# Kernel optimization log

Hardware: AMD Instinct MI355X
Metric: run time of the kernel (lower is better)

The kernel has to match this reference:

```python
import jax, jax.numpy as jnp
import numpy as np

N = 50000   # nodes
E = 600000  # edges
D = 128     # node_input_dim
H = 128     # hidden_dim
A = 200000  # number of valid actions


def setup_inputs() -> dict:
    key = jax.random.key(0)
    ks = jax.random.split(key, 8)
    x = jax.random.normal(ks[0], (N, D), dtype=jnp.float32)
    edge_index = jax.random.randint(ks[1], (2, E), 0, N, dtype=jnp.int64)
    valid_actions = jax.random.randint(ks[2], (A, 2), 0, N, dtype=jnp.int64)
    # GCNConv uses glorot-style init for weight, zeros/uniform for bias; exact init is irrelevant for correctness
    s1 = 1.0 / np.sqrt(D)
    sH = 1.0 / np.sqrt(H)
    s2 = 1.0 / np.sqrt(2 * H)
    W1 = jax.random.uniform(ks[3], (D, H), jnp.float32, -s1, s1)
    b1 = jax.random.uniform(ks[4], (H,), jnp.float32, -s1, s1)
    W2 = jax.random.uniform(ks[5], (H, H), jnp.float32, -sH, sH)
    b2 = jax.random.uniform(ks[6], (H,), jnp.float32, -sH, sH)
    Wq = jax.random.uniform(ks[7], (2 * H, 1), jnp.float32, -s2, s2)
    bq = jnp.zeros((1,), jnp.float32)
    return {"x": x, "edge_index": edge_index, "valid_actions": valid_actions,
            "W1": W1, "b1": b1, "W2": W2, "b2": b2, "Wq": Wq, "bq": bq}


def _gcn_conv(h, src, dst, norm, W, b, n_nodes):
    # PyG GCNConv: x' = D^{-1/2} (A + I) D^{-1/2} X W + b
    h = h @ W                              # [N, H]
    msg = h[src] * norm[:, None]           # [E+N, H] gather + scale
    out = jax.ops.segment_sum(msg, dst, num_segments=n_nodes)  # scatter-add
    return out + b


def reference(x, edge_index, valid_actions, W1, b1, W2, b2, Wq, bq):
    n = x.shape[0]
    loops = jnp.arange(n, dtype=edge_index.dtype)
    src = jnp.concatenate([edge_index[0], loops])  # self-loops appended
    dst = jnp.concatenate([edge_index[1], loops])
    # symmetric normalization from in-degree of A+I (unit edge weights)
    deg = jax.ops.segment_sum(jnp.ones_like(dst, x.dtype), dst, num_segments=n)
    dis = jnp.where(deg > 0, jax.lax.rsqrt(deg), 0.0)
    norm = dis[src] * dis[dst]             # [E+N]

    h = jax.nn.relu(_gcn_conv(x, src, dst, norm, W1, b1, n))
    h = jax.nn.relu(_gcn_conv(h, src, dst, norm, W2, b2, n))

    # batched gather-concat-linear replacing the per-action Python loop
    pair = jnp.concatenate([h[valid_actions[:, 0]], h[valid_actions[:, 1]]], axis=-1)  # [A, 2H]
    q = pair @ Wq + bq                     # [A, 1]
    return q.reshape(-1)                   # torch.cat of A scalars -> [A]
```

## Files before the change

kernel.cpp:

```cpp
#include <hip/hip_runtime.h>
#include <hip/hip_bf16.h>

#define HDIM 128

typedef __attribute__((ext_vector_type(8))) short bf16x8_t;
typedef __attribute__((ext_vector_type(4))) float f32x4_t;

__device__ inline unsigned short bf16_rne(float x) {
    union { __hip_bfloat16 b; unsigned short u; } cv;
    cv.b = __float2bfloat16(x);
    return cv.u;
}
__device__ inline void split2(float x, unsigned short& h, unsigned short& l) {
    h = bf16_rne(x);
    l = bf16_rne(x - __uint_as_float((unsigned int)h << 16));
}

__global__ void deg_count_k(const int* __restrict__ dst, int* __restrict__ deg, int E) {
    int i = blockIdx.x * blockDim.x + threadIdx.x;
    if (i < E) atomicAdd(&deg[dst[i]], 1);
}

__global__ void scan_part_k(const int* __restrict__ deg, int* __restrict__ incl,
                            int* __restrict__ blocksum, int N) {
    __shared__ int s[256];
    const int tid = threadIdx.x;
    const int i = blockIdx.x * 256 + tid;
    int v = (i < N) ? deg[i] : 0;
    s[tid] = v;
    __syncthreads();
    #pragma unroll
    for (int off = 1; off < 256; off <<= 1) {
        int t = (tid >= off) ? s[tid - off] : 0;
        __syncthreads();
        s[tid] += t;
        __syncthreads();
    }
    if (i < N) incl[i] = s[tid];
    if (tid == 255) blocksum[blockIdx.x] = s[255];
}

__global__ void scan_final_k(const int* __restrict__ deg, const int* __restrict__ incl,
                             const int* __restrict__ blocksum, int* __restrict__ rowptr,
                             float* __restrict__ dis, int N, int E, int NB) {
    __shared__ int s[256];
    const int tid = threadIdx.x, bid = blockIdx.x;
    const int i = bid * 256 + tid;
    const int v = (tid < NB) ? blocksum[tid] : 0;
    s[tid] = v;
    __syncthreads();
    #pragma unroll
    for (int off = 1; off < 256; off <<= 1) {
        int t = (tid >= off) ? s[tid - off] : 0;
        __syncthreads();
        s[tid] += t;
        __syncthreads();
    }
    const int excl = s[bid] - blocksum[bid];
    if (i < N) {
        rowptr[i] = excl + incl[i] - deg[i];
        dis[i] = rsqrtf((float)deg[i] + 1.0f);
    }
    if (i == 0) rowptr[N] = E;
}

__global__ void fill_csr_k(const int* __restrict__ src, const int* __restrict__ dst,
                           const int* __restrict__ rowptr, int* __restrict__ cursor,
                           int* __restrict__ csr, int E) {
    int e = blockIdx.x * blockDim.x + threadIdx.x;
    if (e < E) {
        const int d = dst[e];
        const int pos = rowptr[d] + atomicAdd(&cursor[d], 1);
        csr[pos] = src[e];
    }
}

__global__ void pack_w2_k(const float* __restrict__ W1, const float* __restrict__ W2,
                          unsigned short* __restrict__ Wp1, unsigned short* __restrict__ Wp2) {
    const int idx = blockIdx.x * 256 + threadIdx.x;
    const float* W = (idx < 16384) ? W1 : W2;
    unsigned short* hi = (idx < 16384) ? Wp1 : Wp2;
    const int id = idx & 16383;
    const int frag = id >> 9;
    const int r = id & 511;
    const int lane = r >> 3, j = r & 7;
    const int c = frag & 7, sfrag = frag >> 3;
    const int col = (c << 4) | (lane & 15);
    const int k = (sfrag << 5) + ((lane >> 4) << 3) + j;
    unsigned short h, l;
    split2(W[k * HDIM + col], h, l);
    hi[id] = h;
    hi[id + 16384] = l;
}

__global__ __launch_bounds__(512, 4) void mfma_gemm_k(
    const float* __restrict__ X, const unsigned short* __restrict__ Wp,
    const float* __restrict__ dis, float* __restrict__ hs, int N) {
    __shared__ __align__(16) unsigned short wlds[32768];
    const int tid = threadIdx.x;
    {
        const float4* wsrc = reinterpret_cast<const float4*>(Wp);
        float4* wdst = reinterpret_cast<float4*>(wlds);
        #pragma unroll
        for (int i = 0; i < 8; ++i) wdst[tid + i * 512] = wsrc[tid + i * 512];
    }
    __syncthreads();

    const int wave = tid >> 6, lane = tid & 63;
    const int row0 = (blockIdx.x << 7) + (wave << 4);
    if (row0 >= N) return;
    const int lrow = lane & 15;
    const int kgrp = (lane >> 4) << 3;

    const long abase = ((long)(row0 + lrow) << 7) + kgrp;

    f32x4_t acc[8];
    #pragma unroll
    for (int c = 0; c < 8; ++c) acc[c] = (f32x4_t){0.f, 0.f, 0.f, 0.f};

    #pragma unroll
    for (int s = 0; s < 4; ++s) {
        const float4 a0 = *reinterpret_cast<const float4*>(X + abase + (s << 5));
        const float4 a1 = *reinterpret_cast<const float4*>(X + abase + (s << 5) + 4);
        const float xv[8] = {a0.x, a0.y, a0.z, a0.w, a1.x, a1.y, a1.z, a1.w};
        bf16x8_t ah, al;
        #pragma unroll
        for (int j = 0; j < 8; ++j) {
            unsigned short h, l;
            split2(xv[j], h, l);
            ah[j] = (short)h;
            al[j] = (short)l;
        }
        #pragma unroll
        for (int c = 0; c < 8; ++c) {
            const int fo = (((s << 3) + c) << 9) + (lane << 3);
            const bf16x8_t bh = *reinterpret_cast<const bf16x8_t*>(wlds + fo);
            const bf16x8_t bl = *reinterpret_cast<const bf16x8_t*>(wlds + 16384 + fo);
            acc[c] = __builtin_amdgcn_mfma_f32_16x16x32_bf16(ah, bh, acc[c], 0, 0, 0);
            acc[c] = __builtin_amdgcn_mfma_f32_16x16x32_bf16(al, bh, acc[c], 0, 0, 0);
            acc[c] = __builtin_amdgcn_mfma_f32_16x16x32_bf16(ah, bl, acc[c], 0, 0, 0);
        }
    }

    const int rbase = row0 + ((lane >> 4) << 2);
    float d[4];
    #pragma unroll
    for (int i = 0; i < 4; ++i) d[i] = dis[rbase + i];
    #pragma unroll
    for (int c = 0; c < 8; ++c) {
        const int col = (c << 4) | lrow;
        #pragma unroll
        for (int i = 0; i < 4; ++i)
            hs[((long)(rbase + i) << 7) + col] = acc[c][i] * d[i];
    }
}

template<bool PROJ>
__global__ __launch_bounds__(256) void gather_agg_k(
    const int* __restrict__ rowptr, const int* __restrict__ csr,
    const float* __restrict__ hs, const float* __restrict__ dis,
    const float* __restrict__ b, float* __restrict__ o,
    const float* __restrict__ Wq, float* __restrict__ pu, float* __restrict__ pv, int N) {
    const int lane = threadIdx.x & 63;
    const int wid = (int)((blockIdx.x * (long)blockDim.x + threadIdx.x) >> 6);
    const int nw = (int)(((long)gridDim.x * blockDim.x) >> 6);
    const float2 bb = *reinterpret_cast<const float2*>(&b[lane * 2]);
    float2 wu = {0.f, 0.f}, wv = {0.f, 0.f};
    if constexpr (PROJ) {
        wu = *reinterpret_cast<const float2*>(&Wq[lane * 2]);
        wv = *reinterpret_cast<const float2*>(&Wq[HDIM + lane * 2]);
    }
    const int loff = lane * 2;
    for (int n = wid; n < N; n += nw) {
        const int r0 = rowptr[n], r1 = rowptr[n + 1];
        float2 acc = *reinterpret_cast<const float2*>(&hs[((long)n << 7) + loff]);
        float2 acc2 = {0.f, 0.f};
        int e = r0;
        for (; e + 8 <= r1; e += 8) {
            const int s0 = csr[e],     s1 = csr[e + 1], s2 = csr[e + 2], s3 = csr[e + 3];
            const int s4 = csr[e + 4], s5 = csr[e + 5], s6 = csr[e + 6], s7 = csr[e + 7];
            const float2 v0 = *reinterpret_cast<const float2*>(&hs[((long)s0 << 7) + loff]);
            const float2 v1 = *reinterpret_cast<const float2*>(&hs[((long)s1 << 7) + loff]);
            const float2 v2 = *reinterpret_cast<const float2*>(&hs[((long)s2 << 7) + loff]);
            const float2 v3 = *reinterpret_cast<const float2*>(&hs[((long)s3 << 7) + loff]);
            const float2 v4 = *reinterpret_cast<const float2*>(&hs[((long)s4 << 7) + loff]);
            const float2 v5 = *reinterpret_cast<const float2*>(&hs[((long)s5 << 7) + loff]);
            const float2 v6 = *reinterpret_cast<const float2*>(&hs[((long)s6 << 7) + loff]);
            const float2 v7 = *reinterpret_cast<const float2*>(&hs[((long)s7 << 7) + loff]);
            acc.x  += v0.x + v1.x;  acc.y  += v0.y + v1.y;
            acc2.x += v2.x + v3.x;  acc2.y += v2.y + v3.y;
            acc.x  += v4.x + v5.x;  acc.y  += v4.y + v5.y;
            acc2.x += v6.x + v7.x;  acc2.y += v6.y + v7.y;
        }
        for (; e + 2 <= r1; e += 2) {
            const int s0 = csr[e], s1 = csr[e + 1];
            const float2 v0 = *reinterpret_cast<const float2*>(&hs[((long)s0 << 7) + loff]);
            const float2 v1 = *reinterpret_cast<const float2*>(&hs[((long)s1 << 7) + loff]);
            acc.x += v0.x + v1.x;
            acc.y += v0.y + v1.y;
        }
        if (e < r1) {
            const int s0 = csr[e];
            const float2 v0 = *reinterpret_cast<const float2*>(&hs[((long)s0 << 7) + loff]);
            acc.x += v0.x;
            acc.y += v0.y;
        }
        acc.x += acc2.x;
        acc.y += acc2.y;
        const float dv = dis[n];
        const float o0 = fmaxf(fmaf(acc.x, dv, bb.x), 0.f);
        const float o1 = fmaxf(fmaf(acc.y, dv, bb.y), 0.f);
        if constexpr (!PROJ) {
            float2 ov = {o0, o1};
            *reinterpret_cast<float2*>(o + ((long)n << 7) + loff) = ov;
        } else {
            float su = o0 * wu.x + o1 * wu.y;
            float sv = o0 * wv.x + o1 * wv.y;
            #pragma unroll
            for (int off = 32; off > 0; off >>= 1) {
                su += __shfl_down(su, off, 64);
                sv += __shfl_down(sv, off, 64);
            }
            if (lane == 0) {
                pu[n] = su;
                pv[n] = sv;
            }
        }
    }
}

__global__ __launch_bounds__(256) void qhead_k(
    const float* __restrict__ pu, const float* __restrict__ pv,
    const int* __restrict__ va, const float* __restrict__ bq,
    float* __restrict__ out, int A) {
    const float bqv = bq[0];
    int i = blockIdx.x * blockDim.x + threadIdx.x;
    const int stride = gridDim.x * blockDim.x;
    for (; i < A; i += stride) {
        const int2 uv = reinterpret_cast<const int2*>(va)[i];
        out[i] = pu[uv.x] + pv[uv.y] + bqv;
    }
}

extern "C" void kernel_launch(void* const* d_in, const int* in_sizes, int n_in,
                              void* d_out, int out_size, void* d_ws, size_t ws_size,
                              hipStream_t stream) {
    const float* x   = (const float*)d_in[0];
    const int*   ei  = (const int*)d_in[1];
    const int*   va  = (const int*)d_in[2];
    const float* W1  = (const float*)d_in[3];
    const float* b1  = (const float*)d_in[4];
    const float* W2  = (const float*)d_in[5];
    const float* b2  = (const float*)d_in[6];
    const float* Wq  = (const float*)d_in[7];
    const float* bq  = (const float*)d_in[8];
    float* out = (float*)d_out;

    const int N = in_sizes[0] / HDIM;
    const int E = in_sizes[1] / 2;
    const int A = in_sizes[2] / 2;
    const int* esrc = ei;
    const int* edst = ei + E;

    const int Nal = (N + 63) & ~63;

    char* p = (char*)d_ws;
    auto alloc = [&](size_t bytes) { char* r = p; p += (bytes + 255) & ~(size_t)255; return r; };
    int* deg_i    = (int*)alloc((size_t)Nal * 4 * 2);
    int* cursor   = deg_i + Nal;
    int* incl     = (int*)alloc((size_t)N * 4);
    int* rowptr   = (int*)alloc((size_t)(N + 1) * 4);
    int* blocksum = (int*)alloc(256 * 4);
    int* csr      = (int*)alloc((size_t)E * 4);
    float* dis    = (float*)alloc((size_t)N * 4);
    float* pu     = (float*)alloc((size_t)N * 4);
    float* pv     = (float*)alloc((size_t)N * 4);
    unsigned short* Wp1 = (unsigned short*)alloc(32768 * 2);
    unsigned short* Wp2 = (unsigned short*)alloc(32768 * 2);
    float* bufA   = (float*)alloc((size_t)N * HDIM * 4);
    float* bufB   = (float*)alloc((size_t)N * HDIM * 4);

    const int T = 256;
    const int NB = (N + 255) / 256;

    hipMemsetAsync(deg_i, 0, (size_t)Nal * 4 * 2, stream);
    deg_count_k<<<(E + T - 1) / T, T, 0, stream>>>(edst, deg_i, E);
    scan_part_k<<<NB, 256, 0, stream>>>(deg_i, incl, blocksum, N);
    scan_final_k<<<NB, 256, 0, stream>>>(deg_i, incl, blocksum, rowptr, dis, N, E, NB);
    fill_csr_k<<<(E + T - 1) / T, T, 0, stream>>>(esrc, edst, rowptr, cursor, csr, E);

    pack_w2_k<<<128, 256, 0, stream>>>(W1, W2, Wp1, Wp2);

    mfma_gemm_k<<<(N + 127) / 128, 512, 0, stream>>>(x, Wp1, dis, bufA, N);
    gather_agg_k<false><<<2048, T, 0, stream>>>(rowptr, csr, bufA, dis, b1,
                                                bufB, nullptr, nullptr, nullptr, N);

    mfma_gemm_k<<<(N + 127) / 128, 512, 0, stream>>>(bufB, Wp2, dis, bufA, N);
    gather_agg_k<true><<<2048, T, 0, stream>>>(rowptr, csr, bufA, dis, b2,
                                               nullptr, Wq, pu, pv, N);

    qhead_k<<<512, T, 0, stream>>>(pu, pv, va, bq, out, A);
}
```

Before: 269.7 us.

## Fuse layer-1 aggregation with layer-2 GEMM via shared-memory tile

Layer-1 neighbour aggregation (bias plus ReLU) now feeds straight into the layer-2 MFMA GEMM inside one kernel. Each 256-thread block aggregates 16 nodes into shared memory, then multiplies them by the packed W2 using split-bf16 MFMAs. This removes one full N×128 fp32 write and read of the intermediate activations and one kernel launch. In exchange, blocks are small and have a fixed node assignment, which may hurt load balance and latency hiding. The grid of N/16 assumes N is divisible by 16. The gather unroll also drops from 8 to 4 in both gather kernels.

```diff
diff --git a/kernel.cpp b/kernel.cpp
--- a/kernel.cpp
+++ b/kernel.cpp
@@ -155,51 +155,126 @@
     }
 }
 
-template<bool PROJ>
-__global__ __launch_bounds__(256) void gather_agg_k(
+__global__ __launch_bounds__(256) void gather_gemm2_k(
+    const int* __restrict__ rowptr, const int* __restrict__ csr,
+    const float* __restrict__ hs1, const float* __restrict__ dis,
+    const float* __restrict__ b1, const unsigned short* __restrict__ Wp2,
+    float* __restrict__ hs2, int N) {
+    __shared__ __align__(16) float h1[16][132];
+    const int tid = threadIdx.x;
+    const int wave = tid >> 6, lane = tid & 63;
+    const int base = blockIdx.x << 4;
+    const int loff = lane * 2;
+    const float2 bb = *reinterpret_cast<const float2*>(&b1[loff]);
+
+    #pragma unroll
+    for (int i = 0; i < 4; ++i) {
+        const int n = base + (wave << 2) + i;
+        const int r0 = rowptr[n], r1 = rowptr[n + 1];
+        float2 acc = *reinterpret_cast<const float2*>(&hs1[((long)n << 7) + loff]);
+        float2 acc2 = {0.f, 0.f};
+        int e = r0;
+        for (; e + 4 <= r1; e += 4) {
+            const int s0 = csr[e], s1 = csr[e + 1], s2 = csr[e + 2], s3 = csr[e + 3];
+            const float2 v0 = *reinterpret_cast<const float2*>(&hs1[((long)s0 << 7) + loff]);
+            const float2 v1 = *reinterpret_cast<const float2*>(&hs1[((long)s1 << 7) + loff]);
+            const float2 v2 = *reinterpret_cast<const float2*>(&hs1[((long)s2 << 7) + loff]);
+            const float2 v3 = *reinterpret_cast<const float2*>(&hs1[((long)s3 << 7) + loff]);
+            acc.x  += v0.x + v1.x;  acc.y  += v0.y + v1.y;
+            acc2.x += v2.x + v3.x;  acc2.y += v2.y + v3.y;
+        }
+        for (; e < r1; ++e) {
+            const int s0 = csr[e];
+            const float2 v0 = *reinterpret_cast<const float2*>(&hs1[((long)s0 << 7) + loff]);
+            acc.x += v0.x;
+            acc.y += v0.y;
+        }
+        acc.x += acc2.x;
+        acc.y += acc2.y;
+        const float dv = dis[n];
+        const int r = (wave << 2) + i;
+        h1[r][loff]     = fmaxf(fmaf(acc.x, dv, bb.x), 0.f);
+        h1[r][loff + 1] = fmaxf(fmaf(acc.y, dv, bb.y), 0.f);
+    }
+    __syncthreads();
+
+    const int lrow = lane & 15;
+    const int kgrp = (lane >> 4) << 3;
+    f32x4_t acc0 = (f32x4_t){0.f, 0.f, 0.f, 0.f};
+    f32x4_t acc1 = (f32x4_t){0.f, 0.f, 0.f, 0.f};
+    const int c0 = wave << 1;
+
+    #pragma unroll
+    for (int s = 0; s < 4; ++s) {
+        const float4 a0 = *reinterpret_cast<const float4*>(&h1[lrow][kgrp + (s << 5)]);
+        const float4 a1 = *reinterpret_cast<const float4*>(&h1[lrow][kgrp + (s << 5) + 4]);
+        const float xv[8] = {a0.x, a0.y, a0.z, a0.w, a1.x, a1.y, a1.z, a1.w};
+        bf16x8_t ah, al;
+        #pragma unroll
+        for (int j = 0; j < 8; ++j) {
+            unsigned short h, l;
+            split2(xv[j], h, l);
+            ah[j] = (short)h;
+            al[j] = (short)l;
+        }
+        {
+            const int fo = (((s << 3) + c0) << 9) + (lane << 3);
+            const bf16x8_t bh = *reinterpret_cast<const bf16x8_t*>(Wp2 + fo);
+            const bf16x8_t bl = *reinterpret_cast<const bf16x8_t*>(Wp2 + 16384 + fo);
+            acc0 = __builtin_amdgcn_mfma_f32_16x16x32_bf16(ah, bh, acc0, 0, 0, 0);
+            acc0 = __builtin_amdgcn_mfma_f32_16x16x32_bf16(al, bh, acc0, 0, 0, 0);
+            acc0 = __builtin_amdgcn_mfma_f32_16x16x32_bf16(ah, bl, acc0, 0, 0, 0);
+        }
+        {
+            const int fo = (((s << 3) + c0 + 1) << 9) + (lane << 3);
+            const bf16x8_t bh = *reinterpret_cast<const bf16x8_t*>(Wp2 + fo);
+            const bf16x8_t bl = *reinterpret_cast<const bf16x8_t*>(Wp2 + 16384 + fo);
+            acc1 = __builtin_amdgcn_mfma_f32_16x16x32_bf16(ah, bh, acc1, 0, 0, 0);
+            acc1 = __builtin_amdgcn_mfma_f32_16x16x32_bf16(al, bh, acc1, 0, 0, 0);
+            acc1 = __builtin_amdgcn_mfma_f32_16x16x32_bf16(ah, bl, acc1, 0, 0, 0);
+        }
+    }
+
+    const int rb = base + ((lane >> 4) << 2);
+    float d[4];
+    #pragma unroll
+    for (int i = 0; i < 4; ++i) d[i] = dis[rb + i];
+    const int col0 = (c0 << 4) | lrow;
+    const int col1 = ((c0 + 1) << 4) | lrow;
+    #pragma unroll
+    for (int i = 0; i < 4; ++i) {
+        hs2[((long)(rb + i) << 7) + col0] = acc0[i] * d[i];
+        hs2[((long)(rb + i) << 7) + col1] = acc1[i] * d[i];
+    }
+}
+
+__global__ __launch_bounds__(256) void gather_proj_k(
     const int* __restrict__ rowptr, const int* __restrict__ csr,
     const float* __restrict__ hs, const float* __restrict__ dis,
-    const float* __restrict__ b, float* __restrict__ o,
-    const float* __restrict__ Wq, float* __restrict__ pu, float* __restrict__ pv, int N) {
+    const float* __restrict__ b, const float* __restrict__ Wq,
+    float* __restrict__ pu, float* __restrict__ pv, int N) {
     const int lane = threadIdx.x & 63;
     const int wid = (int)((blockIdx.x * (long)blockDim.x + threadIdx.x) >> 6);
     const int nw = (int)(((long)gridDim.x * blockDim.x) >> 6);
     const float2 bb = *reinterpret_cast<const float2*>(&b[lane * 2]);
-    float2 wu = {0.f, 0.f}, wv = {0.f, 0.f};
-    if constexpr (PROJ) {
-        wu = *reinterpret_cast<const float2*>(&Wq[lane * 2]);
-        wv = *reinterpret_cast<const float2*>(&Wq[HDIM + lane * 2]);
-    }
+    const float2 wu = *reinterpret_cast<const float2*>(&Wq[lane * 2]);
+    const float2 wv = *reinterpret_cast<const float2*>(&Wq[HDIM + lane * 2]);
     const int loff = lane * 2;
     for (int n = wid; n < N; n += nw) {
         const int r0 = rowptr[n], r1 = rowptr[n + 1];
         float2 acc = *reinterpret_cast<const float2*>(&hs[((long)n << 7) + loff]);
         float2 acc2 = {0.f, 0.f};
         int e = r0;
-        for (; e + 8 <= r1; e += 8) {
-            const int s0 = csr[e],     s1 = csr[e + 1], s2 = csr[e + 2], s3 = csr[e + 3];
-            const int s4 = csr[e + 4], s5 = csr[e + 5], s6 = csr[e + 6], s7 = csr[e + 7];
+        for (; e + 4 <= r1; e += 4) {
+            const int s0 = csr[e], s1 = csr[e + 1], s2 = csr[e + 2], s3 = csr[e + 3];
             const float2 v0 = *reinterpret_cast<const float2*>(&hs[((long)s0 << 7) + loff]);
             const float2 v1 = *reinterpret_cast<const float2*>(&hs[((long)s1 << 7) + loff]);
             const float2 v2 = *reinterpret_cast<const float2*>(&hs[((long)s2 << 7) + loff]);
             const float2 v3 = *reinterpret_cast<const float2*>(&hs[((long)s3 << 7) + loff]);
-            const float2 v4 = *reinterpret_cast<const float2*>(&hs[((long)s4 << 7) + loff]);
-            const float2 v5 = *reinterpret_cast<const float2*>(&hs[((long)s5 << 7) + loff]);
-            const float2 v6 = *reinterpret_cast<const float2*>(&hs[((long)s6 << 7) + loff]);
-            const float2 v7 = *reinterpret_cast<const float2*>(&hs[((long)s7 << 7) + loff]);
             acc.x  += v0.x + v1.x;  acc.y  += v0.y + v1.y;
             acc2.x += v2.x + v3.x;  acc2.y += v2.y + v3.y;
-            acc.x  += v4.x + v5.x;  acc.y  += v4.y + v5.y;
-            acc2.x += v6.x + v7.x;  acc2.y += v6.y + v7.y;
-        }
-        for (; e + 2 <= r1; e += 2) {
-            const int s0 = csr[e], s1 = csr[e + 1];
-            const float2 v0 = *reinterpret_cast<const float2*>(&hs[((long)s0 << 7) + loff]);
-            const float2 v1 = *reinterpret_cast<const float2*>(&hs[((long)s1 << 7) + loff]);
-            acc.x += v0.x + v1.x;
-            acc.y += v0.y + v1.y;
-        }
-        if (e < r1) {
+        }
+        for (; e < r1; ++e) {
             const int s0 = csr[e];
             const float2 v0 = *reinterpret_cast<const float2*>(&hs[((long)s0 << 7) + loff]);
             acc.x += v0.x;
@@ -210,21 +285,16 @@
         const float dv = dis[n];
         const float o0 = fmaxf(fmaf(acc.x, dv, bb.x), 0.f);
         const float o1 = fmaxf(fmaf(acc.y, dv, bb.y), 0.f);
-        if constexpr (!PROJ) {
-            float2 ov = {o0, o1};
-            *reinterpret_cast<float2*>(o + ((long)n << 7) + loff) = ov;
-        } else {
-            float su = o0 * wu.x + o1 * wu.y;
-            float sv = o0 * wv.x + o1 * wv.y;
-            #pragma unroll
-            for (int off = 32; off > 0; off >>= 1) {
-                su += __shfl_down(su, off, 64);
-                sv += __shfl_down(sv, off, 64);
-            }
-            if (lane == 0) {
-                pu[n] = su;
-                pv[n] = sv;
-            }
+        float su = o0 * wu.x + o1 * wu.y;
+        float sv = o0 * wv.x + o1 * wv.y;
+        #pragma unroll
+        for (int off = 32; off > 0; off >>= 1) {
+            su += __shfl_down(su, off, 64);
+            sv += __shfl_down(sv, off, 64);
+        }
+        if (lane == 0) {
+            pu[n] = su;
+            pv[n] = sv;
         }
     }
 }
@@ -292,12 +362,10 @@
     pack_w2_k<<<128, 256, 0, stream>>>(W1, W2, Wp1, Wp2);
 
     mfma_gemm_k<<<(N + 127) / 128, 512, 0, stream>>>(x, Wp1, dis, bufA, N);
-    gather_agg_k<false><<<2048, T, 0, stream>>>(rowptr, csr, bufA, dis, b1,
-                                                bufB, nullptr, nullptr, nullptr, N);
-
-    mfma_gemm_k<<<(N + 127) / 128, 512, 0, stream>>>(bufB, Wp2, dis, bufA, N);
-    gather_agg_k<true><<<2048, T, 0, stream>>>(rowptr, csr, bufA, dis, b2,
-                                               nullptr, Wq, pu, pv, N);
+
+    gather_gemm2_k<<<N / 16, 256, 0, stream>>>(rowptr, csr, bufA, dis, b1, Wp2, bufB, N);
+
+    gather_proj_k<<<2048, T, 0, stream>>>(rowptr, csr, bufB, dis, b2, Wq, pu, pv, N);
 
     qhead_k<<<512, T, 0, stream>>>(pu, pv, va, bq, out, A);
 }
```

Result: no change. 269.9 us (+0.1%).
